# Kernel tuning notes

Measured on AMD Instinct MI355X. Metric: run time of the kernel, lower is better.

## Reference

```python
import jax, jax.numpy as jnp
import numpy as np

N, D, H, E, K = 16384, 256, 512, 16, 2  # nodes, node_dim, expert hidden, n_experts, active_k
LB_WEIGHT = 0.01
EPS = 1e-5


def setup_inputs() -> dict:
    key = jax.random.key(0)
    k0, k1, k2, k3 = jax.random.split(key, 4)
    x = jax.random.normal(k0, (N, D), jnp.float32)
    # router weight: torch nn.Linear(D, E, bias=False) -> weight [E, D], init std=0.02
    Wr = jax.random.normal(k1, (E, D), jnp.float32) * 0.02
    # stacked expert weights (torch Linear weights transposed to [in, out])
    W1 = jax.random.normal(k2, (E, D, H), jnp.float32) * 0.02
    W2 = jax.random.normal(k3, (E, H, D), jnp.float32) * 0.02
    ln_gamma = jnp.ones((D,), jnp.float32)
    ln_beta = jnp.zeros((D,), jnp.float32)
    return {"x": x, "Wr": Wr, "W1": W1, "W2": W2, "ln_gamma": ln_gamma, "ln_beta": ln_beta}


def reference(x, Wr, W1, W2, ln_gamma, ln_beta):
    n = x.shape[0]
    router_logits = x @ Wr.T                                  # [N, E]
    router_probs = jax.nn.softmax(router_logits, axis=-1)     # [N, E]
    top_w, top_i = jax.lax.top_k(router_probs, K)             # [N, K] each
    top_w = top_w / (top_w.sum(axis=-1, keepdims=True) + 1e-9)
    # dense combine weights: cw[n, e] = renormalized weight if e selected else 0
    cw = jnp.zeros((n, E), x.dtype).at[jnp.arange(n)[:, None], top_i].set(top_w)
    # per-expert FFN on all tokens (fixed-shape dense dispatch), exact-erf GELU like nn.GELU
    h = jax.nn.gelu(jnp.einsum('nd,edh->neh', x, W1), approximate=False)  # [N, E, H]
    y = jnp.einsum('neh,ehd->ned', h, W2)                     # [N, E, D]
    moe_out = jnp.einsum('ne,ned->nd', cw, y)                 # [N, D]
    # residual + LayerNorm
    z = x + moe_out
    mu = z.mean(axis=-1, keepdims=True)
    var = ((z - mu) ** 2).mean(axis=-1, keepdims=True)
    out = (z - mu) / jnp.sqrt(var + EPS) * ln_gamma + ln_beta
    # load-balance loss (counts are non-differentiable, like torch.no_grad())
    counts = jax.ops.segment_sum(jnp.ones((n * K,), router_probs.dtype),
                                 top_i.reshape(-1), num_segments=E)
    frac_tokens = jax.lax.stop_gradient(counts) / (n * K + 1e-9)
    lb_loss = LB_WEIGHT * (E * jnp.sum(frac_tokens * router_probs.mean(axis=0)))
    return out, lb_loss, jax.lax.stop_gradient(router_probs), top_i
```

## Files before the change

kernel.cpp:

```cpp
#include <hip/hip_runtime.h>
#include <hip/hip_bf16.h>
#include <math.h>

#define N_TOK 16384
#define DIM   256
#define HID   512
#define NEXP  16
#define NSLOT (N_TOK * 2)
#define RT    32
#define MAXT  (NSLOT / RT + NEXP)

typedef __attribute__((ext_vector_type(8))) short bf16x8;
typedef __attribute__((ext_vector_type(4))) float f32x4;
#define MFMA(a, b, c) __builtin_amdgcn_mfma_f32_16x16x32_bf16(a, b, c, 0, 0, 0)

__device__ __forceinline__ unsigned short f2b(float f) {
  union { float f; unsigned int i; } c; c.f = f;
  unsigned int r = c.i + 0x7FFFu + ((c.i >> 16) & 1u);
  return (unsigned short)(r >> 16);
}

__device__ __forceinline__ float gelu_f(float v) {
  float v2 = v * v;
  float u2 = v * fmaf(0.10294322f, v2, 2.3022082f);
  float s  = __builtin_amdgcn_exp2f(u2);
  float r  = __builtin_amdgcn_rcpf(1.0f + s);
  return fmaf(-v, r, v);
}

__global__ __launch_bounds__(256) void prep_kernel(
    const float* __restrict__ W1, const float* __restrict__ W2,
    unsigned short* __restrict__ W1f, unsigned short* __restrict__ W2f)
{
  int id = blockIdx.x * 256 + threadIdx.x;
  if (id < 524288) {
    int i4 = id * 4;
    int inner = i4 & 31;
    int h  = (i4 >> 5) & 511;
    int kb = (i4 >> 14) & 7;
    int e  = i4 >> 17;
    const float* src = W1 + ((size_t)(e * 256 + kb * 32 + inner) * 512 + h);
    ushort4 o;
    o.x = f2b(src[0]); o.y = f2b(src[512]); o.z = f2b(src[1024]); o.w = f2b(src[1536]);
    *(ushort4*)(W1f + i4) = o;
  } else {
    int i4 = (id - 524288) * 4;
    int inner = i4 & 31;
    int d2 = (i4 >> 5) & 255;
    int kb = (i4 >> 13) & 15;
    int e  = i4 >> 17;
    const float* src = W2 + ((size_t)(e * 512 + kb * 32 + inner) * 256 + d2);
    ushort4 o;
    o.x = f2b(src[0]); o.y = f2b(src[256]); o.z = f2b(src[512]); o.w = f2b(src[768]);
    *(ushort4*)(W2f + i4) = o;
  }
}

__global__ __launch_bounds__(256) void router_kernel(
    const float* __restrict__ x, const float* __restrict__ Wr,
    float* __restrict__ probs_out, float* __restrict__ topi_out,
    float* __restrict__ topw, int* __restrict__ sel, float* __restrict__ g_partial,
    unsigned short* __restrict__ xb)
{
  __shared__ float sp[16];
  int tid = threadIdx.x;
  int wv = tid >> 6, lane = tid & 63;
  int tok = blockIdx.x * 4 + wv;
  int e = lane & 15, q = lane >> 4;
  if (tid < 16) sp[tid] = 0.f;
  __syncthreads();

  const float4* xr = (const float4*)(x + (size_t)tok * DIM + q * 64);
  const float4* wr = (const float4*)(Wr + (size_t)e * DIM + q * 64);
  float a0 = 0.f, a1 = 0.f, a2 = 0.f, a3 = 0.f;
  #pragma unroll
  for (int i = 0; i < 16; ++i) {
    float4 xa = xr[i], wa = wr[i];
    a0 += xa.x * wa.x; a1 += xa.y * wa.y; a2 += xa.z * wa.z; a3 += xa.w * wa.w;
  }
  float lg = (a0 + a1) + (a2 + a3);
  lg += __shfl_xor(lg, 16, 64);
  lg += __shfl_xor(lg, 32, 64);

  float mx = lg;
  #pragma unroll
  for (int o = 1; o < 16; o <<= 1) mx = fmaxf(mx, __shfl_xor(mx, o, 64));
  float ex = expf(lg - mx);
  float ssum = ex;
  #pragma unroll
  for (int o = 1; o < 16; o <<= 1) ssum += __shfl_xor(ssum, o, 64);
  float p = ex / ssum;

  if (lane < 16) {
    probs_out[(size_t)tok * NEXP + e] = p;
    atomicAdd(&sp[e], p);
  }

  {
    float4 xc = *(const float4*)(x + (size_t)tok * DIM + lane * 4);
    ushort4 o;
    o.x = f2b(xc.x); o.y = f2b(xc.y); o.z = f2b(xc.z); o.w = f2b(xc.w);
    *(ushort4*)(xb + (size_t)tok * DIM + lane * 4) = o;
  }

  float p1 = p; int i1 = e;
  #pragma unroll
  for (int o = 1; o < 16; o <<= 1) {
    float po = __shfl_xor(p1, o, 64); int io = __shfl_xor(i1, o, 64);
    if (po > p1 || (po == p1 && io < i1)) { p1 = po; i1 = io; }
  }
  float pm = (e == i1) ? -1.f : p;
  float p2 = pm; int i2 = e;
  #pragma unroll
  for (int o = 1; o < 16; o <<= 1) {
    float po = __shfl_xor(p2, o, 64); int io = __shfl_xor(i2, o, 64);
    if (po > p2 || (po == p2 && io < i2)) { p2 = po; i2 = io; }
  }
  if (lane == 0) {
    float rs = 1.0f / (p1 + p2 + 1e-9f);
    int s0 = tok * 2;
    topw[s0] = p1 * rs;  topw[s0 + 1] = p2 * rs;
    sel[s0] = i1;        sel[s0 + 1] = i2;
    topi_out[s0] = (float)i1;  topi_out[s0 + 1] = (float)i2;
  }
  __syncthreads();
  if (tid < 16) g_partial[(size_t)tid * 4096 + blockIdx.x] = sp[tid];
}

__global__ __launch_bounds__(256) void scatter_kernel(
    const int* __restrict__ sel, const float* __restrict__ topw,
    int* __restrict__ cursors, int* __restrict__ tok_of_pos, float* __restrict__ w_of_pos)
{
  __shared__ int bcnt[16];
  __shared__ int bbase[16];
  int tid = threadIdx.x;
  if (tid < 16) bcnt[tid] = 0;
  __syncthreads();
  int s = blockIdx.x * 256 + tid;
  int e = sel[s];
  int my = atomicAdd(&bcnt[e], 1);
  __syncthreads();
  if (tid < 16) bbase[tid] = atomicAdd(&cursors[tid], bcnt[tid]);
  __syncthreads();
  int idx = e * NSLOT + bbase[e] + my;
  tok_of_pos[idx] = s >> 1;
  w_of_pos[idx]   = topw[s];
}

__global__ __launch_bounds__(1024) void stats_kernel(
    const int* __restrict__ cursors, const float* __restrict__ g_partial,
    int* __restrict__ perm, float* __restrict__ lb_out)
{
  __shared__ float sp[16];
  __shared__ int nt[16];
  __shared__ int P[9];
  int tid = threadIdx.x;
  int wv = tid >> 6, lane = tid & 63;
  float sacc = 0.f;
  #pragma unroll
  for (int j = 0; j < 64; ++j) sacc += g_partial[(size_t)wv * 4096 + j * 64 + lane];
  #pragma unroll
  for (int o = 32; o; o >>= 1) sacc += __shfl_xor(sacc, o, 64);
  if (lane == 0) sp[wv] = sacc;
  if (tid < 16) nt[tid] = (cursors[tid] + RT - 1) / RT;
  __syncthreads();

  if (tid == 0) {
    float acc = 0.f;
    for (int e = 0; e < NEXP; ++e)
      acc += ((float)cursors[e] / (32768.0f + 1e-9f)) * (sp[e] * (1.0f / 16384.0f));
    lb_out[0] = 0.01f * 16.0f * acc;
    int pp = 0;
    for (int g = 0; g < 8; ++g) { P[g] = pp; pp += nt[g] + nt[g + 8]; }
    P[8] = pp;
  }
  __syncthreads();

  for (int t = tid; t < MAXT; t += 1024) {
    int g = 0;
    #pragma unroll
    for (int gg = 1; gg < 8; ++gg) if (t >= P[gg]) g = gg;
    int v = -1;
    if (t < P[8]) {
      int r = t - P[g];
      int e = (r < nt[g]) ? g : g + 8;
      int mt = (r < nt[g]) ? r : r - nt[g];
      v = (e << 16) | mt;
    }
    perm[t] = v;
  }
}

__global__ __launch_bounds__(512, 4) void ffn_kernel(
    const unsigned short* __restrict__ xb,
    const unsigned short* __restrict__ W1f, const unsigned short* __restrict__ W2f,
    const int* __restrict__ cursors, const int* __restrict__ perm,
    const int* __restrict__ tok_of_pos, const float* __restrict__ w_of_pos,
    float* __restrict__ zbuf)
{
  __shared__ __align__(16) unsigned short As[8 * 32 * 32];
  __shared__ __align__(16) unsigned short Hs[16 * 32 * 32];
  __shared__ float rwS[RT];
  __shared__ int   tokS[RT];

  int b = blockIdx.x;
  int rr = (b & 7) * (MAXT / 8) + (b >> 3);
  int pv = perm[rr];
  if (pv < 0) return;
  int e = pv >> 16, mtile = pv & 0xFFFF;
  int cnt = cursors[e];
  int base = e * NSLOT;
  int m0 = mtile * RT;

  int tid = threadIdx.x;
  if (tid < RT) {
    int rl = m0 + tid;
    tokS[tid] = (rl < cnt) ? tok_of_pos[base + rl] : -1;
    rwS[tid]  = (rl < cnt) ? w_of_pos[base + rl] : 0.f;
  }
  __syncthreads();

  #pragma unroll
  for (int q = 0; q < 2; ++q) {
    int idx = q * 512 + tid;
    int row = idx >> 5, cb = idx & 31;
    int tk = tokS[row];
    bf16x8 v = {0, 0, 0, 0, 0, 0, 0, 0};
    if (tk >= 0) v = *(const bf16x8*)(xb + (size_t)tk * DIM + cb * 8);
    *(bf16x8*)&As[(cb >> 2) * 1024 + (cb & 3) * 8 + row * 32] = v;
  }
  __syncthreads();

  int lane = tid & 63;
  int w = tid >> 6;
  int l15 = lane & 15, g = lane >> 4;

  bf16x8 af[2][8];
  #pragma unroll
  for (int mf = 0; mf < 2; ++mf)
    #pragma unroll
    for (int kb = 0; kb < 8; ++kb)
      af[mf][kb] = *(bf16x8*)&As[kb * 1024 + (mf * 16 + l15) * 32 + g * 8];

  const unsigned short* W1e = W1f + (size_t)e * (8 * 512 * 32);
  #pragma unroll
  for (int cf = 0; cf < 4; ++cf) {
    int col0 = w * 64 + cf * 16;
    f32x4 ac0 = {0.f, 0.f, 0.f, 0.f}, ac1 = {0.f, 0.f, 0.f, 0.f};
    #pragma unroll
    for (int kb = 0; kb < 8; ++kb) {
      bf16x8 bfr = *(const bf16x8*)(W1e + (size_t)(kb * 512 + col0 + l15) * 32 + g * 8);
      ac0 = MFMA(af[0][kb], bfr, ac0);
      ac1 = MFMA(af[1][kb], bfr, ac1);
    }
    int col = col0 + l15;
    int kbo = (col >> 5) * 1024 + (col & 31);
    #pragma unroll
    for (int reg = 0; reg < 4; ++reg) {
      int row0 = g * 4 + reg;
      Hs[kbo + row0 * 32]        = f2b(gelu_f(ac0[reg]));
      Hs[kbo + (row0 + 16) * 32] = f2b(gelu_f(ac1[reg]));
    }
  }
  __syncthreads();

  const unsigned short* W2e = W2f + (size_t)e * (16 * 256 * 32);
  #pragma unroll
  for (int cf = 0; cf < 2; ++cf) {
    int col0 = w * 32 + cf * 16;
    bf16x8 bfr[16];
    #pragma unroll
    for (int kb = 0; kb < 16; ++kb)
      bfr[kb] = *(const bf16x8*)(W2e + (size_t)(kb * 256 + col0 + l15) * 32 + g * 8);

    #pragma unroll
    for (int mf = 0; mf < 2; ++mf) {
      f32x4 ac = {0.f, 0.f, 0.f, 0.f};
      #pragma unroll
      for (int kb = 0; kb < 16; ++kb) {
        bf16x8 hfr = *(bf16x8*)&Hs[kb * 1024 + (mf * 16 + l15) * 32 + g * 8];
        ac = MFMA(hfr, bfr[kb], ac);
      }
      int col = col0 + l15;
      #pragma unroll
      for (int reg = 0; reg < 4; ++reg) {
        int row = mf * 16 + g * 4 + reg;
        int t = tokS[row];
        if (t >= 0) atomicAdd(zbuf + (size_t)t * DIM + col, ac[reg] * rwS[row]);
      }
    }
  }
}

__global__ __launch_bounds__(256) void combine_ln_kernel(
    const float* __restrict__ x, const float* __restrict__ zbuf,
    const float* __restrict__ gamma, const float* __restrict__ beta,
    float* __restrict__ outp)
{
  int wv = threadIdx.x >> 6, lane = threadIdx.x & 63;
  int tok = blockIdx.x * 4 + wv;
  int d0 = lane << 2;
  float4 xv = *(const float4*)(x + (size_t)tok * DIM + d0);
  float4 mv = *(const float4*)(zbuf + (size_t)tok * DIM + d0);
  float z0 = xv.x + mv.x, z1 = xv.y + mv.y, z2 = xv.z + mv.z, z3 = xv.w + mv.w;
  float s = z0 + z1 + z2 + z3;
  float q = z0 * z0 + z1 * z1 + z2 * z2 + z3 * z3;
  #pragma unroll
  for (int off = 32; off > 0; off >>= 1) {
    s += __shfl_xor(s, off, 64);
    q += __shfl_xor(q, off, 64);
  }
  float mu  = s * (1.0f / 256.0f);
  float var = q * (1.0f / 256.0f) - mu * mu;
  float inv = rsqrtf(var + 1e-5f);
  float4 gv = *(const float4*)(gamma + d0);
  float4 bv = *(const float4*)(beta + d0);
  float4 ov;
  ov.x = (z0 - mu) * inv * gv.x + bv.x;
  ov.y = (z1 - mu) * inv * gv.y + bv.y;
  ov.z = (z2 - mu) * inv * gv.z + bv.z;
  ov.w = (z3 - mu) * inv * gv.w + bv.w;
  *(float4*)(outp + (size_t)tok * DIM + d0) = ov;
}

extern "C" void kernel_launch(void* const* d_in, const int* in_sizes, int n_in,
                              void* d_out, int out_size, void* d_ws, size_t ws_size,
                              hipStream_t stream)
{
  const float* x     = (const float*)d_in[0];
  const float* Wr    = (const float*)d_in[1];
  const float* W1    = (const float*)d_in[2];
  const float* W2    = (const float*)d_in[3];
  const float* gamma = (const float*)d_in[4];
  const float* beta  = (const float*)d_in[5];

  float* ob = (float*)d_out;
  float* out_main  = ob;
  float* lb_out    = ob + (size_t)N_TOK * DIM;
  float* probs_out = ob + (size_t)N_TOK * DIM + 1;
  float* topi_out  = ob + (size_t)N_TOK * DIM + 1 + (size_t)N_TOK * NEXP;

  char* ws = (char*)d_ws;
  int*   cursors    = (int*)(ws + 0);
  int*   perm       = (int*)(ws + 1024);
  float* g_partial  = (float*)(ws + 65536);
  float* topw       = (float*)(ws + 327680);
  int*   sel        = (int*)(ws + 458752);
  int*   tok_of_pos = (int*)(ws + 589824);
  float* w_of_pos   = (float*)(ws + 2686976);
  unsigned short* xb  = (unsigned short*)(ws + 4980736);
  unsigned short* W1f = (unsigned short*)(ws + 13369344);
  unsigned short* W2f = (unsigned short*)(ws + 17563648);
  float* zbuf       = (float*)(ws + 21757952);

  hipMemsetAsync(cursors, 0, 64, stream);
  hipMemsetAsync(zbuf, 0, (size_t)N_TOK * DIM * 4, stream);
  prep_kernel<<<4096, 256, 0, stream>>>(W1, W2, W1f, W2f);
  router_kernel<<<N_TOK / 4, 256, 0, stream>>>(x, Wr, probs_out, topi_out, topw, sel, g_partial, xb);
  scatter_kernel<<<NSLOT / 256, 256, 0, stream>>>(sel, topw, cursors, tok_of_pos, w_of_pos);
  stats_kernel<<<1, 1024, 0, stream>>>(cursors, g_partial, perm, lb_out);
  ffn_kernel<<<MAXT, 512, 0, stream>>>(xb, W1f, W2f, cursors, perm, tok_of_pos, w_of_pos, zbuf);
  combine_ln_kernel<<<N_TOK / 4, 256, 0, stream>>>(x, zbuf, gamma, beta, out_main);
}
```

Baseline: 243.2 us.

## Double FFN row tile, swizzle LDS, fold stats and zbuf clear into scatter

The FFN row tile grows from 32 to 64 tokens per block, so each W1/W2 fragment load feeds twice as many MFMAs. The As/Hs LDS layouts are XOR-swizzled to reduce bank conflicts, and launch bounds are relaxed because the larger tile needs more registers and LDS. The stats kernel is merged into scatter through a last-block-done atomic counter, and zeroing zbuf moves into scatter so the memset goes away. The cost is fewer, heavier FFN blocks with lower occupancy, plus a serialized tail in the last scatter block.

```diff
diff --git a/kernel.cpp b/kernel.cpp
--- a/kernel.cpp
+++ b/kernel.cpp
@@ -7,8 +7,9 @@
 #define HID   512
 #define NEXP  16
 #define NSLOT (N_TOK * 2)
-#define RT    32
+#define RT    64
 #define MAXT  (NSLOT / RT + NEXP)
+#define XCDC  (MAXT / 8)
 
 typedef __attribute__((ext_vector_type(8))) short bf16x8;
 typedef __attribute__((ext_vector_type(4))) float f32x4;
@@ -129,7 +130,10 @@
 
 __global__ __launch_bounds__(256) void scatter_kernel(
     const int* __restrict__ sel, const float* __restrict__ topw,
-    int* __restrict__ cursors, int* __restrict__ tok_of_pos, float* __restrict__ w_of_pos)
+    const float* __restrict__ g_partial,
+    int* __restrict__ cursors, int* __restrict__ gdone,
+    int* __restrict__ tok_of_pos, float* __restrict__ w_of_pos,
+    float* __restrict__ zbuf, int* __restrict__ perm, float* __restrict__ lb_out)
 {
   __shared__ int bcnt[16];
   __shared__ int bbase[16];
@@ -145,66 +149,78 @@
   int idx = e * NSLOT + bbase[e] + my;
   tok_of_pos[idx] = s >> 1;
   w_of_pos[idx]   = topw[s];
-}
-
-__global__ __launch_bounds__(1024) void stats_kernel(
-    const int* __restrict__ cursors, const float* __restrict__ g_partial,
-    int* __restrict__ perm, float* __restrict__ lb_out)
-{
+
+  {
+    float4 zz = {0.f, 0.f, 0.f, 0.f};
+    float4* zp = (float4*)zbuf + (size_t)blockIdx.x * 8192 + tid;
+    #pragma unroll
+    for (int i = 0; i < 32; ++i) zp[i * 256] = zz;
+  }
+
+  __threadfence();
+  __shared__ int lastS;
+  if (tid == 0) lastS = (atomicAdd(gdone, 1) == 127) ? 1 : 0;
+  __syncthreads();
+  if (!lastS) return;
+
   __shared__ float sp[16];
   __shared__ int nt[16];
   __shared__ int P[9];
-  int tid = threadIdx.x;
+  __shared__ int ccnt[16];
   int wv = tid >> 6, lane = tid & 63;
-  float sacc = 0.f;
-  #pragma unroll
-  for (int j = 0; j < 64; ++j) sacc += g_partial[(size_t)wv * 4096 + j * 64 + lane];
-  #pragma unroll
-  for (int o = 32; o; o >>= 1) sacc += __shfl_xor(sacc, o, 64);
-  if (lane == 0) sp[wv] = sacc;
-  if (tid < 16) nt[tid] = (cursors[tid] + RT - 1) / RT;
-  __syncthreads();
-
+  if (tid < 16) ccnt[tid] = atomicAdd(&cursors[tid], 0);
+  #pragma unroll
+  for (int ee = 0; ee < 4; ++ee) {
+    int ex = wv * 4 + ee;
+    float sacc = 0.f;
+    #pragma unroll
+    for (int j = 0; j < 64; ++j) sacc += g_partial[(size_t)ex * 4096 + j * 64 + lane];
+    #pragma unroll
+    for (int o = 32; o; o >>= 1) sacc += __shfl_xor(sacc, o, 64);
+    if (lane == 0) sp[ex] = sacc;
+  }
+  __syncthreads();
+  if (tid < 16) nt[tid] = (ccnt[tid] + RT - 1) / RT;
+  __syncthreads();
   if (tid == 0) {
     float acc = 0.f;
-    for (int e = 0; e < NEXP; ++e)
-      acc += ((float)cursors[e] / (32768.0f + 1e-9f)) * (sp[e] * (1.0f / 16384.0f));
+    for (int e2 = 0; e2 < NEXP; ++e2)
+      acc += ((float)ccnt[e2] / (32768.0f + 1e-9f)) * (sp[e2] * (1.0f / 16384.0f));
     lb_out[0] = 0.01f * 16.0f * acc;
     int pp = 0;
     for (int g = 0; g < 8; ++g) { P[g] = pp; pp += nt[g] + nt[g + 8]; }
     P[8] = pp;
   }
   __syncthreads();
-
-  for (int t = tid; t < MAXT; t += 1024) {
+  for (int t = tid; t < MAXT; t += 256) {
     int g = 0;
     #pragma unroll
     for (int gg = 1; gg < 8; ++gg) if (t >= P[gg]) g = gg;
     int v = -1;
     if (t < P[8]) {
       int r = t - P[g];
-      int e = (r < nt[g]) ? g : g + 8;
+      int e2 = (r < nt[g]) ? g : g + 8;
       int mt = (r < nt[g]) ? r : r - nt[g];
-      v = (e << 16) | mt;
+      v = (e2 << 16) | mt;
     }
     perm[t] = v;
   }
 }
 
-__global__ __launch_bounds__(512, 4) void ffn_kernel(
+__global__ __launch_bounds__(512, 1) void ffn_kernel(
     const unsigned short* __restrict__ xb,
     const unsigned short* __restrict__ W1f, const unsigned short* __restrict__ W2f,
     const int* __restrict__ cursors, const int* __restrict__ perm,
     const int* __restrict__ tok_of_pos, const float* __restrict__ w_of_pos,
     float* __restrict__ zbuf)
 {
-  __shared__ __align__(16) unsigned short As[8 * 32 * 32];
-  __shared__ __align__(16) unsigned short Hs[16 * 32 * 32];
+  __shared__ __align__(16) unsigned short As[8 * 64 * 32];
+  __shared__ __align__(16) unsigned short Hs[16 * 64 * 32];
   __shared__ float rwS[RT];
   __shared__ int   tokS[RT];
 
   int b = blockIdx.x;
-  int rr = (b & 7) * (MAXT / 8) + (b >> 3);
+  int rr = (b & 7) * XCDC + (b >> 3);
   int pv = perm[rr];
   if (pv < 0) return;
   int e = pv >> 16, mtile = pv & 0xFFFF;
@@ -221,13 +237,14 @@
   __syncthreads();
 
   #pragma unroll
-  for (int q = 0; q < 2; ++q) {
+  for (int q = 0; q < 4; ++q) {
     int idx = q * 512 + tid;
     int row = idx >> 5, cb = idx & 31;
     int tk = tokS[row];
     bf16x8 v = {0, 0, 0, 0, 0, 0, 0, 0};
     if (tk >= 0) v = *(const bf16x8*)(xb + (size_t)tk * DIM + cb * 8);
-    *(bf16x8*)&As[(cb >> 2) * 1024 + (cb & 3) * 8 + row * 32] = v;
+    int si = ((cb >> 2) * 2048 + row * 32 + (cb & 3) * 8) ^ ((row & 7) << 3);
+    *(bf16x8*)&As[si] = v;
   }
   __syncthreads();
 
@@ -235,58 +252,67 @@
   int w = tid >> 6;
   int l15 = lane & 15, g = lane >> 4;
 
-  bf16x8 af[2][8];
-  #pragma unroll
-  for (int mf = 0; mf < 2; ++mf)
+  bf16x8 af[4][8];
+  #pragma unroll
+  for (int mf = 0; mf < 4; ++mf) {
+    int row = mf * 16 + l15;
     #pragma unroll
     for (int kb = 0; kb < 8; ++kb)
-      af[mf][kb] = *(bf16x8*)&As[kb * 1024 + (mf * 16 + l15) * 32 + g * 8];
+      af[mf][kb] = *(const bf16x8*)&As[(kb * 2048 + row * 32 + g * 8) ^ ((row & 7) << 3)];
+  }
 
   const unsigned short* W1e = W1f + (size_t)e * (8 * 512 * 32);
   #pragma unroll
   for (int cf = 0; cf < 4; ++cf) {
     int col0 = w * 64 + cf * 16;
-    f32x4 ac0 = {0.f, 0.f, 0.f, 0.f}, ac1 = {0.f, 0.f, 0.f, 0.f};
+    f32x4 ac[4];
+    #pragma unroll
+    for (int mf = 0; mf < 4; ++mf) ac[mf] = (f32x4){0.f, 0.f, 0.f, 0.f};
     #pragma unroll
     for (int kb = 0; kb < 8; ++kb) {
       bf16x8 bfr = *(const bf16x8*)(W1e + (size_t)(kb * 512 + col0 + l15) * 32 + g * 8);
-      ac0 = MFMA(af[0][kb], bfr, ac0);
-      ac1 = MFMA(af[1][kb], bfr, ac1);
+      #pragma unroll
+      for (int mf = 0; mf < 4; ++mf) ac[mf] = MFMA(af[mf][kb], bfr, ac[mf]);
     }
     int col = col0 + l15;
-    int kbo = (col >> 5) * 1024 + (col & 31);
-    #pragma unroll
-    for (int reg = 0; reg < 4; ++reg) {
-      int row0 = g * 4 + reg;
-      Hs[kbo + row0 * 32]        = f2b(gelu_f(ac0[reg]));
-      Hs[kbo + (row0 + 16) * 32] = f2b(gelu_f(ac1[reg]));
-    }
-  }
-  __syncthreads();
-
-  const unsigned short* W2e = W2f + (size_t)e * (16 * 256 * 32);
-  #pragma unroll
-  for (int cf = 0; cf < 2; ++cf) {
-    int col0 = w * 32 + cf * 16;
-    bf16x8 bfr[16];
-    #pragma unroll
-    for (int kb = 0; kb < 16; ++kb)
-      bfr[kb] = *(const bf16x8*)(W2e + (size_t)(kb * 256 + col0 + l15) * 32 + g * 8);
-
-    #pragma unroll
-    for (int mf = 0; mf < 2; ++mf) {
-      f32x4 ac = {0.f, 0.f, 0.f, 0.f};
-      #pragma unroll
-      for (int kb = 0; kb < 16; ++kb) {
-        bf16x8 hfr = *(bf16x8*)&Hs[kb * 1024 + (mf * 16 + l15) * 32 + g * 8];
-        ac = MFMA(hfr, bfr[kb], ac);
-      }
-      int col = col0 + l15;
+    #pragma unroll
+    for (int mf = 0; mf < 4; ++mf) {
       #pragma unroll
       for (int reg = 0; reg < 4; ++reg) {
         int row = mf * 16 + g * 4 + reg;
-        int t = tokS[row];
-        if (t >= 0) atomicAdd(zbuf + (size_t)t * DIM + col, ac[reg] * rwS[row]);
+        int si = ((col >> 5) * 2048 + row * 32 + (col & 31)) ^ ((row & 7) << 3);
+        Hs[si] = f2b(gelu_f(ac[mf][reg]));
+      }
+    }
+  }
+  __syncthreads();
+
+  const unsigned short* W2e = W2f + (size_t)e * (16 * 256 * 32);
+  bf16x8 b2[2][16];
+  #pragma unroll
+  for (int cf = 0; cf < 2; ++cf)
+    #pragma unroll
+    for (int kb = 0; kb < 16; ++kb)
+      b2[cf][kb] = *(const bf16x8*)(W2e + (size_t)(kb * 256 + w * 32 + cf * 16 + l15) * 32 + g * 8);
+
+  #pragma unroll
+  for (int mf = 0; mf < 4; ++mf) {
+    f32x4 ac0 = {0.f, 0.f, 0.f, 0.f}, ac1 = {0.f, 0.f, 0.f, 0.f};
+    int rowa = mf * 16 + l15;
+    #pragma unroll
+    for (int kb = 0; kb < 16; ++kb) {
+      bf16x8 hfr = *(const bf16x8*)&Hs[(kb * 2048 + rowa * 32 + g * 8) ^ ((rowa & 7) << 3)];
+      ac0 = MFMA(hfr, b2[0][kb], ac0);
+      ac1 = MFMA(hfr, b2[1][kb], ac1);
+    }
+    #pragma unroll
+    for (int reg = 0; reg < 4; ++reg) {
+      int row = mf * 16 + g * 4 + reg;
+      int t = tokS[row];
+      if (t >= 0) {
+        float rw = rwS[row];
+        atomicAdd(zbuf + (size_t)t * DIM + w * 32 + l15,      ac0[reg] * rw);
+        atomicAdd(zbuf + (size_t)t * DIM + w * 32 + 16 + l15, ac1[reg] * rw);
       }
     }
   }
@@ -342,6 +368,7 @@
 
   char* ws = (char*)d_ws;
   int*   cursors    = (int*)(ws + 0);
+  int*   gdone      = (int*)(ws + 64);
   int*   perm       = (int*)(ws + 1024);
   float* g_partial  = (float*)(ws + 65536);
   float* topw       = (float*)(ws + 327680);
@@ -353,12 +380,11 @@
   unsigned short* W2f = (unsigned short*)(ws + 17563648);
   float* zbuf       = (float*)(ws + 21757952);
 
-  hipMemsetAsync(cursors, 0, 64, stream);
-  hipMemsetAsync(zbuf, 0, (size_t)N_TOK * DIM * 4, stream);
+  hipMemsetAsync(cursors, 0, 128, stream);
   prep_kernel<<<4096, 256, 0, stream>>>(W1, W2, W1f, W2f);
   router_kernel<<<N_TOK / 4, 256, 0, stream>>>(x, Wr, probs_out, topi_out, topw, sel, g_partial, xb);
-  scatter_kernel<<<NSLOT / 256, 256, 0, stream>>>(sel, topw, cursors, tok_of_pos, w_of_pos);
-  stats_kernel<<<1, 1024, 0, stream>>>(cursors, g_partial, perm, lb_out);
+  scatter_kernel<<<NSLOT / 256, 256, 0, stream>>>(sel, topw, g_partial, cursors, gdone,
+                                                  tok_of_pos, w_of_pos, zbuf, perm, lb_out);
   ffn_kernel<<<MAXT, 512, 0, stream>>>(xb, W1f, W2f, cursors, perm, tok_of_pos, w_of_pos, zbuf);
   combine_ln_kernel<<<N_TOK / 4, 256, 0, stream>>>(x, zbuf, gamma, beta, out_main);
 }
```

Measured after the change: 225.9 us. -7.1%, faster.
